# Kernel optimization log

Measured on AMD Instinct MI355X. Metric: run time of the kernel, lower is better.

## Reference

```python
import jax, jax.numpy as jnp
import numpy as np

C1, C2, K, R = 32, 16, 3, 2
N, H, W, D = 2, 32, 32, 32


def _conv3d(x, w, b, pad):
    y = jax.lax.conv_general_dilated(
        x, w, window_strides=(1, 1, 1), padding=[(pad, pad)] * 3,
        dimension_numbers=('NCDHW', 'OIDHW', 'NCDHW'))
    return y + b[None, :, None, None, None]


def setup_inputs() -> dict:
    key = jax.random.key(0)
    ks = jax.random.split(key, 4)
    def winit(k, sh, fan):
        return jax.random.normal(k, sh, jnp.float32) * (1.0 / np.sqrt(fan))
    cm = C1 // 4
    ck = R ** 3 * K ** 3
    return {
        'x': jax.random.normal(ks[0], (N, C1, H, W, D), jnp.float32),
        'w_down': winit(ks[1], (cm, C1, 1, 1, 1), C1),
        'b_down': jnp.zeros((cm,), jnp.float32),
        'w_enc': winit(ks[2], (ck, cm, K, K, K), cm * K ** 3),
        'b_enc': jnp.zeros((ck,), jnp.float32),
        'w_out': winit(ks[3], (C2, C1, 1, 1, 1), C1),
        'b_out': jnp.zeros((C2,), jnp.float32),
    }


def reference(x, w_down, b_down, w_enc, b_enc, w_out, b_out):
    k3, r3 = K ** 3, R ** 3
    n, c, h, wd, d = x.shape
    # kernel prediction branch
    t = _conv3d(x, w_down, b_down, 0)                       # [N, C/4, H, W, D]
    enc = _conv3d(t, w_enc, b_enc, K // 2)                  # [N, r^3*k^3, H, W, D]
    # pixel_shuffle(k^3 outer, r^3 inner) + softmax over k^3 + unfold-back == this:
    kern = enc.reshape(n, k3, r3, h, wd, d)
    kern = jax.nn.softmax(kern, axis=1)
    kern = kern.transpose(0, 3, 4, 5, 1, 2)                 # [N, H, W, D, k^3, r^3]
    # im2col of x, same flattening order as torch triple unfold (kh outer, kd inner)
    p = K // 2
    xp = jnp.pad(x, ((0, 0), (0, 0), (p, p), (p, p), (p, p)))
    patches = jnp.stack(
        [xp[:, :, i:i + h, j:j + wd, l:l + d]
         for i in range(K) for j in range(K) for l in range(K)],
        axis=-1)                                            # [N, C, H, W, D, k^3]
    out = jnp.einsum('nchwdk,nhwdkr->nchwdr', patches, kern)  # [N, C, H, W, D, r^3]
    # pixel shuffle 3D (channel layout: C outer, r^3 inner)
    out = out.reshape(n, c, h, wd, d, R, R, R)
    out = out.transpose(0, 1, 2, 5, 3, 6, 4, 7).reshape(n, c, h * R, wd * R, d * R)
    return _conv3d(out, w_out, b_out, 0)                    # [N, C2, H*R, W*R, D*R]
```

## Files before the change

kernel.cpp:

```cpp
#include <hip/hip_runtime.h>


typedef short bf16x8 __attribute__((ext_vector_type(8)));
typedef float f32x4 __attribute__((ext_vector_type(4)));

#define PSTR 232

__device__ inline float b2f(unsigned short u) {
  union { unsigned int i; float f; } x;
  x.i = ((unsigned int)u) << 16;
  return x.f;
}
__device__ inline unsigned short f2b(float f) {
  union { float f; unsigned int i; } x;
  x.f = f;
  unsigned int u = x.i;
  return (unsigned short)((u + 0x7FFFu + ((u >> 16) & 1u)) >> 16);
}
__device__ inline float2 bpair(unsigned int u) {
  union { unsigned int i; float f; } lo, hi;
  lo.i = u << 16;
  hi.i = u & 0xFFFF0000u;
  return make_float2(lo.f, hi.f);
}

__global__ __launch_bounds__(256) void setup_kernel(
    const float* __restrict__ x, const float* __restrict__ w_down,
    const float* __restrict__ b_down, const float* __restrict__ w_enc,
    const float* __restrict__ b_enc, const float* __restrict__ w_out,
    unsigned short* __restrict__ t, unsigned short* __restrict__ xo,
    unsigned short* __restrict__ Wb) {
  int blk = blockIdx.x;
  if (blk < 256) {
    int idx = blk * 256 + threadIdx.x;
    int n = idx >> 15;
    int p = idx & 32767;
    const float* xp = x + ((size_t)n << 20) + p;
    float at[8];
    float ao[16];
#pragma unroll
    for (int m = 0; m < 8; ++m) at[m] = b_down[m];
#pragma unroll
    for (int o = 0; o < 16; ++o) ao[o] = 0.f;
#pragma unroll
    for (int c = 0; c < 32; ++c) {
      float xv = xp[(size_t)c << 15];
#pragma unroll
      for (int m = 0; m < 8; ++m) at[m] = fmaf(xv, w_down[m * 32 + c], at[m]);
#pragma unroll
      for (int o = 0; o < 16; ++o) ao[o] = fmaf(xv, w_out[o * 32 + c], ao[o]);
    }
#pragma unroll
    for (int m = 0; m < 8; ++m) t[(((size_t)n * 8 + m) << 15) + p] = f2b(at[m]);
#pragma unroll
    for (int o = 0; o < 16; ++o) xo[(((size_t)n * 16 + o) << 15) + p] = f2b(ao[o]);
  } else {
    int i = (blk - 256) * 256 + threadIdx.x;
    if (i < 224 * 224) {
      int o = i / 224;
      int k = i - o * 224;
      float v = 0.f;
      if (o < 216) {
        if (k < 216) v = w_enc[o * 216 + k];
        else if (k == 216) v = b_enc[o];
      }
      Wb[i] = f2b(v);
    }
  }
}

__global__ __launch_bounds__(256, 4) void carafe_kernel(
    const unsigned short* __restrict__ tg, const unsigned short* __restrict__ xog,
    const unsigned short* __restrict__ Wb, const float* __restrict__ b_out,
    float* __restrict__ y) {
  __shared__ unsigned short t_lds[1728];
  __shared__ __align__(16) unsigned short p_lds[64 * PSTR];
  __shared__ unsigned short xo_lds[16 * 216];

  int b = blockIdx.x;
  int n = b >> 9;
  int tile = b & 511;
  int h0 = ((tile >> 6) & 7) << 2;
  int w0 = ((tile >> 3) & 7) << 2;
  int d0 = (tile & 7) << 2;
  int tid = threadIdx.x;

  for (int i = tid; i < 1728; i += 256) {
    int m = i / 216;
    int rem = i - m * 216;
    int z = rem / 36;
    int r2 = rem - z * 36;
    int yy = r2 / 6;
    int xx = r2 - yy * 6;
    int gh = h0 + z - 1, gw = w0 + yy - 1, gd = d0 + xx - 1;
    unsigned short val = 0;
    if ((unsigned)gh < 32u && (unsigned)gw < 32u && (unsigned)gd < 32u)
      val = tg[(((size_t)n * 8 + m) << 15) + (gh << 10) + (gw << 5) + gd];
    t_lds[i] = val;
  }
  for (int i = tid; i < 3456; i += 256) {
    int c = i / 216;
    int rem = i - c * 216;
    int z = rem / 36;
    int r2 = rem - z * 36;
    int yy = r2 / 6;
    int xx = r2 - yy * 6;
    int gh = h0 + z - 1, gw = w0 + yy - 1, gd = d0 + xx - 1;
    unsigned short val = 0;
    if ((unsigned)gh < 32u && (unsigned)gw < 32u && (unsigned)gd < 32u)
      val = xog[(((size_t)n * 16 + c) << 15) + (gh << 10) + (gw << 5) + gd];
    xo_lds[i] = val;
  }
  __syncthreads();

  for (int i = tid; i < 7168; i += 256) {
    int v = i / 112;
    int kk = (i - v * 112) * 2;
    int vz = v >> 4, vy = (v >> 2) & 3, vx = v & 3;
    unsigned int pk = 0;
#pragma unroll
    for (int h = 0; h < 2; ++h) {
      int k = kk + h;
      unsigned short val = 0;
      if (k < 216) {
        int m = k / 27;
        int r = k - m * 27;
        int kh = r / 9;
        int r2 = r - kh * 9;
        int kw = r2 / 3;
        int kd = r2 - kw * 3;
        val = t_lds[m * 216 + (vz + kh) * 36 + (vy + kw) * 6 + (vx + kd)];
      } else if (k == 216) {
        val = 0x3F80;
      }
      pk |= ((unsigned int)val) << (16 * h);
    }
    *(unsigned int*)&p_lds[v * PSTR + kk] = pk;
  }
  __syncthreads();

  int lane = tid & 63;
  int wv = __builtin_amdgcn_readfirstlane(tid >> 6);
  int l15 = lane & 15;
  int quad = lane >> 4;
  int mh = wv >> 1;
  int nh = wv & 1;

  f32x4 acc[7][2];
#pragma unroll
  for (int i = 0; i < 7; ++i)
#pragma unroll
    for (int j = 0; j < 2; ++j) acc[i][j] = (f32x4){0.f, 0.f, 0.f, 0.f};
  {
    const unsigned short* Arow = Wb + (mh * 112 + l15) * 224 + quad * 8;
    const unsigned short* Bp = p_lds + (nh * 32 + l15) * PSTR + quad * 8;
#pragma unroll
    for (int kt = 0; kt < 7; ++kt) {
      bf16x8 bf0 = *(const bf16x8*)(Bp + kt * 32);
      bf16x8 bf1 = *(const bf16x8*)(Bp + 16 * PSTR + kt * 32);
#pragma unroll
      for (int i = 0; i < 7; ++i) {
        bf16x8 af = *(const bf16x8*)(Arow + i * 16 * 224 + kt * 32);
        acc[i][0] = __builtin_amdgcn_mfma_f32_16x16x32_bf16(af, bf0, acc[i][0], 0, 0, 0);
        acc[i][1] = __builtin_amdgcn_mfma_f32_16x16x32_bf16(af, bf1, acc[i][1], 0, 0, 0);
      }
    }
  }
  __syncthreads();

#pragma unroll
  for (int i = 0; i < 7; ++i) {
    int o_base = (mh * 7 + i) * 16 + quad * 4;
#pragma unroll
    for (int r = 0; r < 4; r += 2) {
      int o = o_base + r;
      if (o < 216) {
#pragma unroll
        for (int jn = 0; jn < 2; ++jn) {
          int vv = nh * 32 + jn * 16 + l15;
          unsigned int pk = (unsigned int)f2b(acc[i][jn][r]) |
                            ((unsigned int)f2b(acc[i][jn][r + 1]) << 16);
          *(unsigned int*)&p_lds[vv * PSTR + o] = pk;
        }
      }
    }
  }
  __syncthreads();

#pragma unroll
  for (int pp = 0; pp < 2; ++pp) {
    int p = tid + pp * 256;
    int r = p & 7;
    int vv = p >> 3;
    unsigned short* e = p_lds + vv * PSTR + r;
    float vals[27];
    float mx = -3.0e38f;
#pragma unroll
    for (int k = 0; k < 27; ++k) {
      vals[k] = b2f(e[k * 8]);
      mx = fmaxf(mx, vals[k]);
    }
    float s = 0.f;
#pragma unroll
    for (int k = 0; k < 27; ++k) {
      vals[k] = __expf(vals[k] - mx);
      s += vals[k];
    }
    float inv = 1.0f / s;
#pragma unroll
    for (int k = 0; k < 27; ++k) e[k * 8] = f2b(vals[k] * inv);
  }
  __syncthreads();

  int v = tid & 63;
  int vz = v >> 4, vy = (v >> 2) & 3, vx = v & 3;
  int base = vz * 36 + vy * 6 + vx;
  int c2b = wv * 4;
  float2 accy[4][4];
#pragma unroll
  for (int i = 0; i < 4; ++i) {
    float bo = b_out[c2b + i];
#pragma unroll
    for (int j = 0; j < 4; ++j) accy[i][j] = make_float2(bo, bo);
  }
  const unsigned short* kb = p_lds + v * PSTR;
#pragma unroll
  for (int k = 0; k < 27; ++k) {
    int kh = k / 9;
    int r2 = k - kh * 9;
    int kw = r2 / 3;
    int kd = r2 - kw * 3;
    int off = base + kh * 36 + kw * 6 + kd;
    uint4 kw4 = *(const uint4*)(kb + k * 8);
    float2 kr[4];
    kr[0] = bpair(kw4.x);
    kr[1] = bpair(kw4.y);
    kr[2] = bpair(kw4.z);
    kr[3] = bpair(kw4.w);
#pragma unroll
    for (int i = 0; i < 4; ++i) {
      float xv = b2f(xo_lds[(c2b + i) * 216 + off]);
#pragma unroll
      for (int j = 0; j < 4; ++j) {
        accy[i][j].x = fmaf(xv, kr[j].x, accy[i][j].x);
        accy[i][j].y = fmaf(xv, kr[j].y, accy[i][j].y);
      }
    }
  }

  int hh = (h0 + vz) << 1, ww = (w0 + vy) << 1, dd = (d0 + vx) << 1;
#pragma unroll
  for (int i = 0; i < 4; ++i) {
    size_t cb = ((size_t)(n * 16 + c2b + i)) << 18;
#pragma unroll
    for (int rh = 0; rh < 2; ++rh)
#pragma unroll
      for (int rw = 0; rw < 2; ++rw)
        *(float2*)&y[cb + (size_t)((hh + rh) << 12) + ((ww + rw) << 6) + dd] =
            accy[i][rh * 2 + rw];
  }
}

extern "C" void kernel_launch(void* const* d_in, const int* in_sizes, int n_in,
                              void* d_out, int out_size, void* d_ws, size_t ws_size,
                              hipStream_t stream) {
  const float* x      = (const float*)d_in[0];
  const float* w_down = (const float*)d_in[1];
  const float* b_down = (const float*)d_in[2];
  const float* w_enc  = (const float*)d_in[3];
  const float* b_enc  = (const float*)d_in[4];
  const float* w_out  = (const float*)d_in[5];
  const float* b_out  = (const float*)d_in[6];
  float* y = (float*)d_out;

  char* ws = (char*)d_ws;
  unsigned short* t  = (unsigned short*)(ws);
  unsigned short* xo = (unsigned short*)(ws + (1u << 20));
  unsigned short* Wb = (unsigned short*)(ws + (3u << 20));

  setup_kernel<<<dim3(452), dim3(256), 0, stream>>>(x, w_down, b_down, w_enc,
                                                    b_enc, w_out, t, xo, Wb);
  carafe_kernel<<<dim3(1024), dim3(256), 0, stream>>>(t, xo, Wb, b_out, y);
}
```

Before: 141.0 us.

## Store padded halo layouts in workspace and vectorize tile loads and im2col

The setup kernel now writes t and the 1x1-conv output into zero-padded spatial layouts, with the 16 output channels packed as bf16 pairs. The carafe kernel can then load its halo tiles with wide unconditional vector loads instead of per-element bounds checks. Im2col is restructured so each thread builds a packed row segment in registers. Softmax handles two channel pairs per thread through 32-bit LDS accesses, and the reassembly loop uses packed float2 FMAs. Block indices are remapped to improve locality along d. This adds a workspace-zeroing kernel launch and a larger padded workspace.

```diff
diff --git a/kernel.cpp b/kernel.cpp
--- a/kernel.cpp
+++ b/kernel.cpp
@@ -3,8 +3,13 @@
 
 typedef short bf16x8 __attribute__((ext_vector_type(8)));
 typedef float f32x4 __attribute__((ext_vector_type(4)));
+typedef float v2f __attribute__((ext_vector_type(2)));
 
 #define PSTR 232
+#define PSTRD 116
+#define MSP 41616
+#define HSP 1224
+#define WSP 36
 
 __device__ inline float b2f(unsigned short u) {
   union { unsigned int i; float f; } x;
@@ -17,27 +22,31 @@
   unsigned int u = x.i;
   return (unsigned short)((u + 0x7FFFu + ((u >> 16) & 1u)) >> 16);
 }
-__device__ inline float2 bpair(unsigned int u) {
+__device__ inline v2f b2f2(unsigned int u) {
   union { unsigned int i; float f; } lo, hi;
   lo.i = u << 16;
   hi.i = u & 0xFFFF0000u;
-  return make_float2(lo.f, hi.f);
+  return (v2f){lo.f, hi.f};
+}
+
+__global__ __launch_bounds__(256) void zero_ws(uint4* __restrict__ p, int n4) {
+  int i = blockIdx.x * 256 + threadIdx.x;
+  if (i < n4) p[i] = make_uint4(0u, 0u, 0u, 0u);
 }
 
 __global__ __launch_bounds__(256) void setup_kernel(
     const float* __restrict__ x, const float* __restrict__ w_down,
     const float* __restrict__ b_down, const float* __restrict__ w_enc,
     const float* __restrict__ b_enc, const float* __restrict__ w_out,
-    unsigned short* __restrict__ t, unsigned short* __restrict__ xo,
+    unsigned short* __restrict__ t, unsigned int* __restrict__ xo32,
     unsigned short* __restrict__ Wb) {
   int blk = blockIdx.x;
   if (blk < 256) {
     int idx = blk * 256 + threadIdx.x;
-    int n = idx >> 15;
-    int p = idx & 32767;
+    int n = idx >> 15, p = idx & 32767;
+    int h = p >> 10, w = (p >> 5) & 31, d = p & 31;
     const float* xp = x + ((size_t)n << 20) + p;
-    float at[8];
-    float ao[16];
+    float at[8], ao[16];
 #pragma unroll
     for (int m = 0; m < 8; ++m) at[m] = b_down[m];
 #pragma unroll
@@ -50,10 +59,13 @@
 #pragma unroll
       for (int o = 0; o < 16; ++o) ao[o] = fmaf(xv, w_out[o * 32 + c], ao[o]);
     }
-#pragma unroll
-    for (int m = 0; m < 8; ++m) t[(((size_t)n * 8 + m) << 15) + p] = f2b(at[m]);
-#pragma unroll
-    for (int o = 0; o < 16; ++o) xo[(((size_t)n * 16 + o) << 15) + p] = f2b(ao[o]);
+    size_t sp = (size_t)(h + 1) * HSP + (size_t)(w + 1) * WSP + (d + 2);
+#pragma unroll
+    for (int m = 0; m < 8; ++m) t[(size_t)(n * 8 + m) * MSP + sp] = f2b(at[m]);
+#pragma unroll
+    for (int cp = 0; cp < 8; ++cp)
+      xo32[(size_t)(n * 8 + cp) * MSP + sp] =
+          (unsigned int)f2b(ao[2 * cp]) | ((unsigned int)f2b(ao[2 * cp + 1]) << 16);
   } else {
     int i = (blk - 256) * 256 + threadIdx.x;
     if (i < 224 * 224) {
@@ -70,77 +82,88 @@
 }
 
 __global__ __launch_bounds__(256, 4) void carafe_kernel(
-    const unsigned short* __restrict__ tg, const unsigned short* __restrict__ xog,
+    const unsigned short* __restrict__ tg, const unsigned int* __restrict__ xog,
     const unsigned short* __restrict__ Wb, const float* __restrict__ b_out,
     float* __restrict__ y) {
-  __shared__ unsigned short t_lds[1728];
   __shared__ __align__(16) unsigned short p_lds[64 * PSTR];
-  __shared__ unsigned short xo_lds[16 * 216];
-
-  int b = blockIdx.x;
-  int n = b >> 9;
-  int tile = b & 511;
-  int h0 = ((tile >> 6) & 7) << 2;
-  int w0 = ((tile >> 3) & 7) << 2;
-  int d0 = (tile & 7) << 2;
+  __shared__ __align__(16) unsigned short t_lds[1728];
+  __shared__ __align__(16) unsigned int xo_lds[1728];
+
+  unsigned int* p32 = (unsigned int*)p_lds;
+  unsigned int* t32 = (unsigned int*)t_lds;
+
+  int pb = blockIdx.x;
+  int G = ((pb >> 5) << 3) | (pb & 7);
+  int q = (pb >> 3) & 3;
+  int n = G >> 7;
+  int h0 = ((G >> 4) & 7) << 2;
+  int w0 = ((G >> 1) & 7) << 2;
+  int d0 = ((G & 1) * 4 + q) << 2;
   int tid = threadIdx.x;
 
-  for (int i = tid; i < 1728; i += 256) {
-    int m = i / 216;
-    int rem = i - m * 216;
-    int z = rem / 36;
-    int r2 = rem - z * 36;
-    int yy = r2 / 6;
-    int xx = r2 - yy * 6;
-    int gh = h0 + z - 1, gw = w0 + yy - 1, gd = d0 + xx - 1;
-    unsigned short val = 0;
-    if ((unsigned)gh < 32u && (unsigned)gw < 32u && (unsigned)gd < 32u)
-      val = tg[(((size_t)n * 8 + m) << 15) + (gh << 10) + (gw << 5) + gd];
-    t_lds[i] = val;
-  }
-  for (int i = tid; i < 3456; i += 256) {
-    int c = i / 216;
-    int rem = i - c * 216;
-    int z = rem / 36;
-    int r2 = rem - z * 36;
-    int yy = r2 / 6;
-    int xx = r2 - yy * 6;
-    int gh = h0 + z - 1, gw = w0 + yy - 1, gd = d0 + xx - 1;
-    unsigned short val = 0;
-    if ((unsigned)gh < 32u && (unsigned)gw < 32u && (unsigned)gd < 32u)
-      val = xog[(((size_t)n * 16 + c) << 15) + (gh << 10) + (gw << 5) + gd];
-    xo_lds[i] = val;
-  }
-  __syncthreads();
-
-  for (int i = tid; i < 7168; i += 256) {
-    int v = i / 112;
-    int kk = (i - v * 112) * 2;
-    int vz = v >> 4, vy = (v >> 2) & 3, vx = v & 3;
-    unsigned int pk = 0;
-#pragma unroll
-    for (int h = 0; h < 2; ++h) {
-      int k = kk + h;
-      unsigned short val = 0;
-      if (k < 216) {
-        int m = k / 27;
-        int r = k - m * 27;
-        int kh = r / 9;
-        int r2 = r - kh * 9;
-        int kw = r2 / 3;
-        int kd = r2 - kw * 3;
-        val = t_lds[m * 216 + (vz + kh) * 36 + (vy + kw) * 6 + (vx + kd)];
-      } else if (k == 216) {
-        val = 0x3F80;
-      }
-      pk |= ((unsigned int)val) << (16 * h);
-    }
-    *(unsigned int*)&p_lds[v * PSTR + kk] = pk;
+  for (int rr = tid; rr < 288; rr += 256) {
+    int m = rr / 36;
+    int rem = rr - m * 36;
+    int z = rem / 6;
+    int yy = rem - z * 6;
+    size_t gsrc = (size_t)(n * 8 + m) * MSP + (size_t)(h0 + z) * HSP +
+                  (size_t)(w0 + yy) * WSP + d0;
+    uint2 l0 = *(const uint2*)(tg + gsrc);
+    uint2 l1 = *(const uint2*)(tg + gsrc + 4);
+    unsigned a = l0.x, b = l0.y, c = l1.x, e = l1.y;
+    int dst = m * 108 + z * 18 + yy * 3;
+    t32[dst] = (a >> 16) | (b << 16);
+    t32[dst + 1] = (b >> 16) | (c << 16);
+    t32[dst + 2] = (c >> 16) | (e << 16);
+  }
+  for (int rr = tid; rr < 288; rr += 256) {
+    int cp = rr / 36;
+    int rem = rr - cp * 36;
+    int z = rem / 6;
+    int yy = rem - z * 6;
+    size_t gsrc = (size_t)(n * 8 + cp) * MSP + (size_t)(h0 + z) * HSP +
+                  (size_t)(w0 + yy) * WSP + d0;
+    uint4 q0 = *(const uint4*)(xog + gsrc);
+    uint4 q1 = *(const uint4*)(xog + gsrc + 4);
+    int dst = cp * 216 + z * 36 + yy * 6;
+    *(uint2*)&xo_lds[dst] = make_uint2(q0.y, q0.z);
+    *(uint2*)&xo_lds[dst + 2] = make_uint2(q0.w, q1.x);
+    *(uint2*)&xo_lds[dst + 4] = make_uint2(q1.y, q1.z);
   }
   __syncthreads();
 
   int lane = tid & 63;
   int wv = __builtin_amdgcn_readfirstlane(tid >> 6);
+
+  {
+    int vloc = lane >> 2, kq = lane & 3;
+    int v = wv * 16 + vloc;
+    int vz = v >> 4, vy = (v >> 2) & 3, vx = v & 3;
+    int base2 = vz * 36 + vy * 6 + vx;
+    unsigned short s[54];
+#pragma unroll
+    for (int mi = 0; mi < 2; ++mi) {
+      int srcb = base2 + (kq * 2 + mi) * 216;
+#pragma unroll
+      for (int kh = 0; kh < 3; ++kh)
+#pragma unroll
+        for (int kw = 0; kw < 3; ++kw)
+#pragma unroll
+          for (int kd = 0; kd < 3; ++kd)
+            s[mi * 27 + kh * 9 + kw * 3 + kd] = t_lds[srcb + kh * 36 + kw * 6 + kd];
+    }
+    unsigned int* pr = p32 + v * PSTRD + kq * 27;
+#pragma unroll
+    for (int j = 0; j < 27; ++j)
+      pr[j] = (unsigned int)s[2 * j] | ((unsigned int)s[2 * j + 1] << 16);
+    if (tid < 64) {
+      unsigned int* r = p32 + tid * PSTRD;
+      r[108] = 0x3F80u;
+      r[109] = 0u; r[110] = 0u; r[111] = 0u;
+    }
+  }
+  __syncthreads();
+
   int l15 = lane & 15;
   int quad = lane >> 4;
   int mh = wv >> 1;
@@ -170,94 +193,96 @@
 
 #pragma unroll
   for (int i = 0; i < 7; ++i) {
-    int o_base = (mh * 7 + i) * 16 + quad * 4;
-#pragma unroll
-    for (int r = 0; r < 4; r += 2) {
-      int o = o_base + r;
-      if (o < 216) {
-#pragma unroll
-        for (int jn = 0; jn < 2; ++jn) {
-          int vv = nh * 32 + jn * 16 + l15;
-          unsigned int pk = (unsigned int)f2b(acc[i][jn][r]) |
-                            ((unsigned int)f2b(acc[i][jn][r + 1]) << 16);
-          *(unsigned int*)&p_lds[vv * PSTR + o] = pk;
+    int o = (mh * 7 + i) * 16 + quad * 4;
+    if (o < 216) {
+#pragma unroll
+      for (int jn = 0; jn < 2; ++jn) {
+        int vv = nh * 32 + jn * 16 + l15;
+        unsigned lo = (unsigned)f2b(acc[i][jn][0]) | ((unsigned)f2b(acc[i][jn][1]) << 16);
+        unsigned hi = (unsigned)f2b(acc[i][jn][2]) | ((unsigned)f2b(acc[i][jn][3]) << 16);
+        *(uint2*)&p_lds[vv * PSTR + o] = make_uint2(lo, hi);
+      }
+    }
+  }
+  __syncthreads();
+
+  {
+    int vv = tid >> 2, rp = tid & 3;
+    unsigned int* e = p32 + vv * PSTRD + rp;
+    float v0[27], v1[27];
+    float mx0 = -3.0e38f, mx1 = -3.0e38f;
+#pragma unroll
+    for (int k = 0; k < 27; ++k) {
+      v2f f = b2f2(e[k * 4]);
+      v0[k] = f.x; v1[k] = f.y;
+      mx0 = fmaxf(mx0, f.x);
+      mx1 = fmaxf(mx1, f.y);
+    }
+    float s0 = 0.f, s1 = 0.f;
+#pragma unroll
+    for (int k = 0; k < 27; ++k) {
+      v0[k] = __expf(v0[k] - mx0);
+      v1[k] = __expf(v1[k] - mx1);
+      s0 += v0[k];
+      s1 += v1[k];
+    }
+    float i0 = 1.0f / s0, i1 = 1.0f / s1;
+#pragma unroll
+    for (int k = 0; k < 27; ++k)
+      e[k * 4] = (unsigned)f2b(v0[k] * i0) | ((unsigned)f2b(v1[k] * i1) << 16);
+  }
+  __syncthreads();
+
+  int v4 = lane;
+  int vz = v4 >> 4, vy = (v4 >> 2) & 3, vx = v4 & 3;
+  int base = vz * 36 + vy * 6 + vx;
+  int cpb = wv * 2;
+  v2f accy[4][4];
+#pragma unroll
+  for (int i = 0; i < 4; ++i) {
+    float bo = b_out[wv * 4 + i];
+#pragma unroll
+    for (int j = 0; j < 4; ++j) accy[i][j] = (v2f){bo, bo};
+  }
+  const unsigned short* kb = p_lds + v4 * PSTR;
+#pragma unroll
+  for (int kh = 0; kh < 3; ++kh)
+#pragma unroll
+    for (int kw = 0; kw < 3; ++kw)
+#pragma unroll
+      for (int kd = 0; kd < 3; ++kd) {
+        int k = kh * 9 + kw * 3 + kd;
+        int off = base + kh * 36 + kw * 6 + kd;
+        uint4 kw4 = *(const uint4*)(kb + k * 8);
+        v2f kr[4];
+        kr[0] = b2f2(kw4.x);
+        kr[1] = b2f2(kw4.y);
+        kr[2] = b2f2(kw4.z);
+        kr[3] = b2f2(kw4.w);
+        v2f x0 = b2f2(xo_lds[(cpb + 0) * 216 + off]);
+        v2f x1 = b2f2(xo_lds[(cpb + 1) * 216 + off]);
+        float xv[4] = {x0.x, x0.y, x1.x, x1.y};
+#pragma unroll
+        for (int i = 0; i < 4; ++i) {
+          v2f xs = (v2f){xv[i], xv[i]};
+#pragma unroll
+          for (int j = 0; j < 4; ++j)
+            accy[i][j] = __builtin_elementwise_fma(xs, kr[j], accy[i][j]);
         }
       }
-    }
-  }
-  __syncthreads();
-
-#pragma unroll
-  for (int pp = 0; pp < 2; ++pp) {
-    int p = tid + pp * 256;
-    int r = p & 7;
-    int vv = p >> 3;
-    unsigned short* e = p_lds + vv * PSTR + r;
-    float vals[27];
-    float mx = -3.0e38f;
-#pragma unroll
-    for (int k = 0; k < 27; ++k) {
-      vals[k] = b2f(e[k * 8]);
-      mx = fmaxf(mx, vals[k]);
-    }
-    float s = 0.f;
-#pragma unroll
-    for (int k = 0; k < 27; ++k) {
-      vals[k] = __expf(vals[k] - mx);
-      s += vals[k];
-    }
-    float inv = 1.0f / s;
-#pragma unroll
-    for (int k = 0; k < 27; ++k) e[k * 8] = f2b(vals[k] * inv);
-  }
-  __syncthreads();
-
-  int v = tid & 63;
-  int vz = v >> 4, vy = (v >> 2) & 3, vx = v & 3;
-  int base = vz * 36 + vy * 6 + vx;
-  int c2b = wv * 4;
-  float2 accy[4][4];
+
+  int hh = (h0 + vz) << 1, ww = (w0 + vy) << 1, dd = (d0 + vx) << 1;
 #pragma unroll
   for (int i = 0; i < 4; ++i) {
-    float bo = b_out[c2b + i];
-#pragma unroll
-    for (int j = 0; j < 4; ++j) accy[i][j] = make_float2(bo, bo);
-  }
-  const unsigned short* kb = p_lds + v * PSTR;
-#pragma unroll
-  for (int k = 0; k < 27; ++k) {
-    int kh = k / 9;
-    int r2 = k - kh * 9;
-    int kw = r2 / 3;
-    int kd = r2 - kw * 3;
-    int off = base + kh * 36 + kw * 6 + kd;
-    uint4 kw4 = *(const uint4*)(kb + k * 8);
-    float2 kr[4];
-    kr[0] = bpair(kw4.x);
-    kr[1] = bpair(kw4.y);
-    kr[2] = bpair(kw4.z);
-    kr[3] = bpair(kw4.w);
-#pragma unroll
-    for (int i = 0; i < 4; ++i) {
-      float xv = b2f(xo_lds[(c2b + i) * 216 + off]);
-#pragma unroll
-      for (int j = 0; j < 4; ++j) {
-        accy[i][j].x = fmaf(xv, kr[j].x, accy[i][j].x);
-        accy[i][j].y = fmaf(xv, kr[j].y, accy[i][j].y);
-      }
-    }
-  }
-
-  int hh = (h0 + vz) << 1, ww = (w0 + vy) << 1, dd = (d0 + vx) << 1;
-#pragma unroll
-  for (int i = 0; i < 4; ++i) {
-    size_t cb = ((size_t)(n * 16 + c2b + i)) << 18;
+    size_t cb = ((size_t)(n * 16 + wv * 4 + i)) << 18;
 #pragma unroll
     for (int rh = 0; rh < 2; ++rh)
 #pragma unroll
-      for (int rw = 0; rw < 2; ++rw)
+      for (int rw = 0; rw < 2; ++rw) {
+        v2f a = accy[i][rh * 2 + rw];
         *(float2*)&y[cb + (size_t)((hh + rh) << 12) + ((ww + rw) << 6) + dd] =
-            accy[i][rh * 2 + rw];
+            make_float2(a.x, a.y);
+      }
   }
 }
 
@@ -274,11 +299,13 @@
   float* y = (float*)d_out;
 
   char* ws = (char*)d_ws;
-  unsigned short* t  = (unsigned short*)(ws);
-  unsigned short* xo = (unsigned short*)(ws + (1u << 20));
-  unsigned short* Wb = (unsigned short*)(ws + (3u << 20));
-
+  unsigned short* t    = (unsigned short*)(ws);
+  unsigned int*   xo32 = (unsigned int*)(ws + 2663424);
+  unsigned short* Wb   = (unsigned short*)(ws + 5326848);
+
+  int n4 = (2 * 2663424) / 16;
+  zero_ws<<<dim3((n4 + 255) / 256), dim3(256), 0, stream>>>((uint4*)ws, n4);
   setup_kernel<<<dim3(452), dim3(256), 0, stream>>>(x, w_down, b_down, w_enc,
-                                                    b_enc, w_out, t, xo, Wb);
-  carafe_kernel<<<dim3(1024), dim3(256), 0, stream>>>(t, xo, Wb, b_out, y);
-}
+                                                    b_enc, w_out, t, xo32, Wb);
+  carafe_kernel<<<dim3(1024), dim3(256), 0, stream>>>(t, xo32, Wb, b_out, y);
+}
```

Result: faster. 115.7 us (-18.0%).
